# Kernel tuning notes

Hardware: AMD Instinct MI355X
Metric: run time of the kernel (lower is better)

## Reference

```python
import jax, jax.numpy as jnp
import numpy as np

D_MODEL = 1024
NHEAD = 16
HEAD_DIM = D_MODEL // NHEAD
MLP_DIM = 4096
ROPE_THETA = 10000.0


def layer_norm(x, g, b, eps=1e-5):
    mu = jnp.mean(x, axis=-1, keepdims=True)
    var = jnp.var(x, axis=-1, keepdims=True)
    return (x - mu) * jax.lax.rsqrt(var + eps) * g + b


def rope_cos_sin(seq_len, dim):
    # lucidrains RotaryEmbedding: inv_freq over even indices, freqs repeated interleaved
    inv_freq = 1.0 / (ROPE_THETA ** (jnp.arange(0, dim, 2, dtype=jnp.float32) / dim))
    t = jnp.arange(seq_len, dtype=jnp.float32)
    freqs = t[:, None] * inv_freq[None, :]            # (S, dim/2)
    freqs = jnp.repeat(freqs, 2, axis=-1)             # (S, dim) interleaved [f0,f0,f1,f1,...]
    return jnp.cos(freqs), jnp.sin(freqs)


def apply_rope(x, cos, sin):
    # x: (B, S, H, D); interleaved rotate_half: (x0,x1) -> (-x1, x0)
    x1 = x[..., ::2]
    x2 = x[..., 1::2]
    rot = jnp.stack([-x2, x1], axis=-1).reshape(x.shape)
    c = cos[None, :, None, :]
    s = sin[None, :, None, :]
    return x * c + rot * s


def setup_inputs() -> dict:
    key = jax.random.key(0)
    ks = jax.random.split(key, 8)
    B, S = 2, 2048
    sc = 1.0 / np.sqrt(D_MODEL)
    inputs = jax.random.normal(ks[0], (B, S, D_MODEL), dtype=jnp.float32)
    return {
        "inputs": inputs,
        "ln1_g": jnp.ones((D_MODEL,), jnp.float32),
        "ln1_b": jnp.zeros((D_MODEL,), jnp.float32),
        "Wq": jax.random.normal(ks[1], (D_MODEL, D_MODEL), jnp.float32) * sc,
        "Wk": jax.random.normal(ks[2], (D_MODEL, D_MODEL), jnp.float32) * sc,
        "Wv": jax.random.normal(ks[3], (D_MODEL, D_MODEL), jnp.float32) * sc,
        "Wo": jax.random.normal(ks[4], (D_MODEL, D_MODEL), jnp.float32) * sc,
        "ln2_g": jnp.ones((D_MODEL,), jnp.float32),
        "ln2_b": jnp.zeros((D_MODEL,), jnp.float32),
        "Wfc2": jax.random.normal(ks[5], (D_MODEL, MLP_DIM), jnp.float32) * sc,
        "bfc2": jnp.zeros((MLP_DIM,), jnp.float32),
        "Wfc3": jax.random.normal(ks[6], (MLP_DIM, D_MODEL), jnp.float32) * (1.0 / np.sqrt(MLP_DIM)),
        "bfc3": jnp.zeros((D_MODEL,), jnp.float32),
    }


def reference(inputs, ln1_g, ln1_b, Wq, Wk, Wv, Wo, ln2_g, ln2_b, Wfc2, bfc2, Wfc3, bfc3):
    B, S, _ = inputs.shape
    x = layer_norm(inputs, ln1_g, ln1_b)
    q = (x @ Wq).reshape(B, S, NHEAD, HEAD_DIM)
    k = (x @ Wk).reshape(B, S, NHEAD, HEAD_DIM)
    v = (x @ Wv).reshape(B, S, NHEAD, HEAD_DIM)
    cos, sin = rope_cos_sin(S, HEAD_DIM)
    q = apply_rope(q, cos, sin)
    k = apply_rope(k, cos, sin)
    scores = jnp.einsum('bqhd,bkhd->bhqk', q, k) / np.sqrt(HEAD_DIM)
    attn = jax.nn.softmax(scores, axis=-1)
    out = jnp.einsum('bhqk,bkhd->bqhd', attn, v).reshape(B, S, D_MODEL)
    out = out @ Wo
    mlp_in = out + inputs
    h = layer_norm(mlp_in, ln2_g, ln2_b)
    h = jax.nn.gelu(h @ Wfc2 + bfc2, approximate=False)
    h = h @ Wfc3 + bfc3
    return h + mlp_in
```

## Files before the change

kernel.cpp:

```cpp
#include <hip/hip_runtime.h>
#include <cstdint>
#include <cstddef>

typedef __bf16 bf16x8 __attribute__((ext_vector_type(8)));
typedef __bf16 bf16x4 __attribute__((ext_vector_type(4)));
typedef float  f32x4  __attribute__((ext_vector_type(4)));
typedef float  f32x16 __attribute__((ext_vector_type(16)));

__device__ __forceinline__ void load16_to_lds(const void* g, void* l) {
  __builtin_amdgcn_global_load_lds(
      (const __attribute__((address_space(1))) void*)g,
      (__attribute__((address_space(3))) void*)l, 16, 0, 0);
}

__global__ __launch_bounds__(256) void transpose_cast(
    const float* __restrict__ src, __bf16* __restrict__ dst, int K, int N)
{
  __shared__ float tile[32][33];
  const int n0 = blockIdx.x * 32, k0 = blockIdx.y * 32;
  const int tx = threadIdx.x, ty = threadIdx.y;
#pragma unroll
  for (int i = 0; i < 32; i += 8)
    tile[ty + i][tx] = src[(size_t)(k0 + ty + i) * N + n0 + tx];
  __syncthreads();
#pragma unroll
  for (int i = 0; i < 32; i += 8)
    dst[(size_t)(n0 + ty + i) * K + k0 + tx] = (__bf16)tile[tx][ty + i];
}

__global__ __launch_bounds__(256) void ln_kernel(
    const float* __restrict__ x, const float* __restrict__ g,
    const float* __restrict__ bta, __bf16* __restrict__ out)
{
  const int row = blockIdx.x;
  const int t = threadIdx.x;
  const float4 v = ((const float4*)(x + (size_t)row * 1024))[t];
  float s  = v.x + v.y + v.z + v.w;
  float ss = v.x * v.x + v.y * v.y + v.z * v.z + v.w * v.w;
#pragma unroll
  for (int o = 32; o > 0; o >>= 1) { s += __shfl_down(s, o); ss += __shfl_down(ss, o); }
  __shared__ float rs[4], rss[4];
  const int w = t >> 6, l = t & 63;
  if (l == 0) { rs[w] = s; rss[w] = ss; }
  __syncthreads();
  s  = rs[0] + rs[1] + rs[2] + rs[3];
  ss = rss[0] + rss[1] + rss[2] + rss[3];
  const float mu = s * (1.0f / 1024.0f);
  const float var = ss * (1.0f / 1024.0f) - mu * mu;
  const float rstd = rsqrtf(var + 1e-5f);
  const float4 gg = ((const float4*)g)[t];
  const float4 bb = ((const float4*)bta)[t];
  __bf16* o = out + (size_t)row * 1024 + t * 4;
  o[0] = (__bf16)((v.x - mu) * rstd * gg.x + bb.x);
  o[1] = (__bf16)((v.y - mu) * rstd * gg.y + bb.y);
  o[2] = (__bf16)((v.z - mu) * rstd * gg.z + bb.z);
  o[3] = (__bf16)((v.w - mu) * rstd * gg.w + bb.w);
}

enum { EPI_BF16 = 0, EPI_RES_F32 = 1, EPI_GELU_BF16 = 2, EPI_BIAS_RES_F32 = 3 };

template <int TM, int EPI>
__global__ __launch_bounds__(256, 2) void gemm_bf16(
    const __bf16* __restrict__ A, const __bf16* __restrict__ Bt,
    __bf16* __restrict__ outb, float* __restrict__ outf,
    const float* __restrict__ bias, const float* __restrict__ res,
    int M, int N, int K)
{
  constexpr int MT = TM / 32;
  __shared__ __bf16 As[TM * 32];
  __shared__ __bf16 Bs[128 * 32];
  const int tid  = threadIdx.x;
  const int lane = tid & 63, w = tid >> 6;
  const int wm = w >> 1, wn = w & 1;
  const int quad = lane >> 4, l16 = lane & 15;
  const int m0 = blockIdx.y * TM, n0 = blockIdx.x * 128;

  f32x4 acc[MT][4] = {};
  const __bf16* Ag = A  + (size_t)m0 * K;
  const __bf16* Bg = Bt + (size_t)n0 * K;

  for (int k0 = 0; k0 < K; k0 += 32) {
#pragma unroll
    for (int r = 0; r < TM / 64; ++r) {
      const int c = r * 256 + tid;
      const int row = c >> 2, cc = (c & 3) * 8;
      load16_to_lds(Ag + (size_t)row * K + k0 + cc, &As[c * 8]);
    }
#pragma unroll
    for (int r = 0; r < 2; ++r) {
      const int c = r * 256 + tid;
      const int row = c >> 2, cc = (c & 3) * 8;
      load16_to_lds(Bg + (size_t)row * K + k0 + cc, &Bs[c * 8]);
    }
    __syncthreads();
    bf16x8 af[MT], bfr[4];
#pragma unroll
    for (int mt = 0; mt < MT; ++mt)
      af[mt] = *(const bf16x8*)&As[(wm * (TM / 2) + mt * 16 + l16) * 32 + quad * 8];
#pragma unroll
    for (int nt = 0; nt < 4; ++nt)
      bfr[nt] = *(const bf16x8*)&Bs[(wn * 64 + nt * 16 + l16) * 32 + quad * 8];
#pragma unroll
    for (int mt = 0; mt < MT; ++mt)
#pragma unroll
      for (int nt = 0; nt < 4; ++nt)
        acc[mt][nt] = __builtin_amdgcn_mfma_f32_16x16x32_bf16(af[mt], bfr[nt], acc[mt][nt], 0, 0, 0);
    __syncthreads();
  }

#pragma unroll
  for (int mt = 0; mt < MT; ++mt) {
#pragma unroll
    for (int nt = 0; nt < 4; ++nt) {
      const int col = n0 + wn * 64 + nt * 16 + l16;
#pragma unroll
      for (int i = 0; i < 4; ++i) {
        const int row = m0 + wm * (TM / 2) + mt * 16 + quad * 4 + i;
        float v = acc[mt][nt][i];
        const size_t idx = (size_t)row * N + col;
        if (EPI == EPI_BF16) {
          outb[idx] = (__bf16)v;
        } else if (EPI == EPI_RES_F32) {
          outf[idx] = v + res[idx];
        } else if (EPI == EPI_GELU_BF16) {
          v += bias[col];
          outb[idx] = (__bf16)(0.5f * v * (1.0f + erff(v * 0.70710678118f)));
        } else {
          v += bias[col];
          outf[idx] = v + res[idx];
        }
      }
    }
  }
}

__global__ __launch_bounds__(256) void rope_qk(
    const __bf16* __restrict__ qkv, __bf16* __restrict__ qr, __bf16* __restrict__ kr)
{
  const int idx = blockIdx.x * 256 + threadIdx.x;
  const int d2 = idx & 31;
  const int h  = (idx >> 5) & 15;
  const int bs = idx >> 9;
  const int s  = bs & 2047;
  const int b  = bs >> 11;
  const float inv_freq = exp2f(-((float)d2 * (1.0f / 32.0f)) * 13.2877123795f);
  const float ang = (float)s * inv_freq;
  const float c = cosf(ang), sn = sinf(ang);
  const __bf16* qp = qkv + (size_t)bs * 3072 + h * 64 + 2 * d2;
  const __bf16* kp = qp + 1024;
  const float q0 = (float)qp[0], q1 = (float)qp[1];
  const float k0 = (float)kp[0], k1 = (float)kp[1];
  const size_t o = ((size_t)(b * 16 + h) * 2048 + s) * 64 + 2 * d2;
  qr[o]     = (__bf16)(q0 * c - q1 * sn);
  qr[o + 1] = (__bf16)(q1 * c + q0 * sn);
  kr[o]     = (__bf16)(k0 * c - k1 * sn);
  kr[o + 1] = (__bf16)(k1 * c + k0 * sn);
}

__global__ __launch_bounds__(256) void v_transpose(
    const __bf16* __restrict__ qkv, __bf16* __restrict__ vt)
{
  __shared__ __bf16 t[64][72];
  const int st = blockIdx.x, h = blockIdx.y, b = blockIdx.z;
  const int tx = threadIdx.x & 63, ty = threadIdx.x >> 6;
  const int s0 = st * 64;
  const __bf16* src = qkv + ((size_t)(b * 2048 + s0)) * 3072 + 2048 + h * 64;
#pragma unroll
  for (int i = 0; i < 64; i += 4)
    t[ty + i][tx] = src[(size_t)(ty + i) * 3072 + tx];
  __syncthreads();
  __bf16* dst = vt + ((size_t)(b * 16 + h) * 64) * 2048 + s0;
#pragma unroll
  for (int i = 0; i < 64; i += 4)
    dst[(size_t)(ty + i) * 2048 + tx] = t[tx][ty + i];
}

__global__ __launch_bounds__(256, 2) void attn_kernel(
    const __bf16* __restrict__ qr, const __bf16* __restrict__ kr,
    const __bf16* __restrict__ vt, __bf16* __restrict__ attn_o)
{
  constexpr int S = 2048, DH = 64, NH = 16, BQ = 128, BKK = 64;
  __shared__ __align__(16) __bf16 smem[24576];
  __bf16* Qs   = smem;
  __bf16* Ksb  = smem + 8192;
  __bf16* Vtsb = smem + 16384;

  const int tid = threadIdx.x;
  const int lane = tid & 63, w = tid >> 6;
  const int l32 = lane & 31, half = lane >> 5;
  const int qt = blockIdx.x, h = blockIdx.y, b = blockIdx.z;
  const int bh = b * NH + h;
  const __bf16* Q  = qr + ((size_t)bh * S + qt * BQ) * DH;
  const __bf16* Kp = kr + (size_t)bh * S * DH;
  const __bf16* Vp = vt + (size_t)bh * DH * S;
  __bf16* Pb = Qs + w * 2048;

#pragma unroll
  for (int r4 = 0; r4 < 4; ++r4) {
    const int c = r4 * 256 + tid;
    const int r = c >> 3, cb = c & 7;
    load16_to_lds(Q + (size_t)r * DH + ((cb ^ (r & 7)) * 8), &Qs[c * 8]);
  }
#pragma unroll
  for (int r2 = 0; r2 < 2; ++r2) {
    const int c = r2 * 256 + tid;
    const int r = c >> 3, cb = c & 7;
    const int cg = (cb ^ (r & 7)) * 8;
    load16_to_lds(Kp + (size_t)r * DH + cg, &Ksb[c * 8]);
    load16_to_lds(Vp + (size_t)r * S + cg, &Vtsb[c * 8]);
  }
  __syncthreads();

  bf16x8 qfB[4];
  {
    const int row = w * 32 + l32;
#pragma unroll
    for (int c = 0; c < 4; ++c)
      qfB[c] = *(const bf16x8*)&Qs[row * 64 + (((2 * c + half) ^ (row & 7)) * 8)];
  }

  float mreg = -3.0e38f, lreg = 0.0f;
  f32x16 oacc[2] = {};

  for (int kt = 0; kt < S / BKK; ++kt) {
    if (kt) __syncthreads();
    const __bf16* Ks  = Ksb  + (kt & 1) * 4096;
    const __bf16* Vts = Vtsb + (kt & 1) * 4096;

    bf16x8 kf[2][4], vf[2][4];
#pragma unroll
    for (int t = 0; t < 2; ++t) {
      const int row = 32 * t + l32;
#pragma unroll
      for (int c = 0; c < 4; ++c)
        kf[t][c] = *(const bf16x8*)&Ks[row * 64 + (((2 * c + half) ^ (l32 & 7)) * 8)];
    }
#pragma unroll
    for (int v = 0; v < 2; ++v) {
      const int row = 32 * v + l32;
#pragma unroll
      for (int c = 0; c < 4; ++c)
        vf[v][c] = *(const bf16x8*)&Vts[row * 64 + (((2 * c + half) ^ (l32 & 7)) * 8)];
    }

    if (kt + 1 < S / BKK) {
      __bf16* Kn = Ksb  + ((kt + 1) & 1) * 4096;
      __bf16* Vn = Vtsb + ((kt + 1) & 1) * 4096;
      const size_t kk1 = (size_t)(kt + 1) * BKK;
#pragma unroll
      for (int r2 = 0; r2 < 2; ++r2) {
        const int c = r2 * 256 + tid;
        const int r = c >> 3, cb = c & 7;
        const int cg = (cb ^ (r & 7)) * 8;
        load16_to_lds(Kp + (kk1 + r) * DH + cg, &Kn[c * 8]);
        load16_to_lds(Vp + (size_t)r * S + kk1 + cg, &Vn[c * 8]);
      }
    }

    f32x16 sa[2] = {};
#pragma unroll
    for (int t = 0; t < 2; ++t)
#pragma unroll
      for (int c = 0; c < 4; ++c)
        sa[t] = __builtin_amdgcn_mfma_f32_32x32x16_bf16(kf[t][c], qfB[c], sa[t], 0, 0, 0);

    float mx = -3.0e38f;
#pragma unroll
    for (int t = 0; t < 2; ++t)
#pragma unroll
      for (int r = 0; r < 16; ++r) { sa[t][r] *= 0.125f; mx = fmaxf(mx, sa[t][r]); }
    mx = fmaxf(mx, __shfl_xor(mx, 32));
    const float mnew = fmaxf(mreg, mx);
    const float alpha = __expf(mreg - mnew);
    mreg = mnew;
    float sum = 0.0f;
#pragma unroll
    for (int t = 0; t < 2; ++t)
#pragma unroll
      for (int r = 0; r < 16; ++r) {
        const float p = __expf(sa[t][r] - mnew);
        sa[t][r] = p;
        sum += p;
      }
    sum += __shfl_xor(sum, 32);
    lreg = lreg * alpha + sum;
#pragma unroll
    for (int v = 0; v < 2; ++v)
#pragma unroll
      for (int r = 0; r < 16; ++r) oacc[v][r] *= alpha;

#pragma unroll
    for (int t = 0; t < 2; ++t)
#pragma unroll
      for (int g = 0; g < 4; ++g) {
        bf16x4 pv;
#pragma unroll
        for (int i = 0; i < 4; ++i) pv[i] = (__bf16)sa[t][4 * g + i];
        const int kc = 4 * t + g;
        *(bf16x4*)&Pb[l32 * 64 + ((kc ^ (l32 & 7)) * 8) + 4 * half] = pv;
      }

    bf16x8 pf[4];
#pragma unroll
    for (int c = 0; c < 4; ++c)
      pf[c] = *(const bf16x8*)&Pb[l32 * 64 + (((2 * c + half) ^ (l32 & 7)) * 8)];
#pragma unroll
    for (int v = 0; v < 2; ++v)
#pragma unroll
      for (int c = 0; c < 4; ++c)
        oacc[v] = __builtin_amdgcn_mfma_f32_32x32x16_bf16(vf[v][c], pf[c], oacc[v], 0, 0, 0);
  }

  const float linv = 1.0f / lreg;
#pragma unroll
  for (int v = 0; v < 2; ++v)
#pragma unroll
    for (int g = 0; g < 4; ++g) {
      bf16x4 ov;
#pragma unroll
      for (int i = 0; i < 4; ++i) ov[i] = (__bf16)(oacc[v][4 * g + i] * linv);
      const int dc = 4 * v + g;
      *(bf16x4*)&Pb[l32 * 64 + ((dc ^ (l32 & 7)) * 8) + 4 * half] = ov;
    }
#pragma unroll
  for (int cc = 0; cc < 4; ++cc) {
    const int c = cc * 64 + lane;
    const int r = c >> 3, g = c & 7;
    const bf16x8 od = *(const bf16x8*)&Pb[r * 64 + ((g ^ (r & 7)) * 8)];
    const int srow = qt * BQ + w * 32 + r;
    *(bf16x8*)&attn_o[((size_t)b * S + srow) * 1024 + h * 64 + g * 8] = od;
  }
}

extern "C" void kernel_launch(void* const* d_in, const int* in_sizes, int n_in,
                              void* d_out, int out_size, void* d_ws, size_t ws_size,
                              hipStream_t stream) {
  const float* inputs = (const float*)d_in[0];
  const float* ln1_g  = (const float*)d_in[1];
  const float* ln1_b  = (const float*)d_in[2];
  const float* Wq     = (const float*)d_in[3];
  const float* Wk     = (const float*)d_in[4];
  const float* Wv     = (const float*)d_in[5];
  const float* Wo     = (const float*)d_in[6];
  const float* ln2_g  = (const float*)d_in[7];
  const float* ln2_b  = (const float*)d_in[8];
  const float* Wfc2   = (const float*)d_in[9];
  const float* bfc2   = (const float*)d_in[10];
  const float* Wfc3   = (const float*)d_in[11];
  const float* bfc3   = (const float*)d_in[12];
  float* out = (float*)d_out;
  char* ws = (char*)d_ws;
  const size_t MB = 1024 * 1024;

  __bf16* Wqkv_t = (__bf16*)(ws);
  __bf16* Wo_t   = (__bf16*)(ws + 6 * MB);
  __bf16* Wfc2_t = (__bf16*)(ws + 8 * MB);
  __bf16* Wfc3_t = (__bf16*)(ws + 16 * MB);
  __bf16* xb     = (__bf16*)(ws + 24 * MB);
  __bf16* attn_o = xb;
  __bf16* qkv    = (__bf16*)(ws + 32 * MB);
  float*  mlp_in = (float*)(ws + 32 * MB);
  __bf16* h2     = (__bf16*)(ws + 48 * MB);
  __bf16* qrb    = (__bf16*)(ws + 56 * MB);
  __bf16* krb    = (__bf16*)(ws + 64 * MB);
  __bf16* vtb    = (__bf16*)(ws + 72 * MB);
  __bf16* hbuf   = (__bf16*)(ws + 56 * MB);

  const dim3 tb(32, 8);
  transpose_cast<<<dim3(32, 32),  tb, 0, stream>>>(Wq,   Wqkv_t,                1024, 1024);
  transpose_cast<<<dim3(32, 32),  tb, 0, stream>>>(Wk,   Wqkv_t + 1024 * 1024,  1024, 1024);
  transpose_cast<<<dim3(32, 32),  tb, 0, stream>>>(Wv,   Wqkv_t + 2048 * 1024,  1024, 1024);
  transpose_cast<<<dim3(32, 32),  tb, 0, stream>>>(Wo,   Wo_t,                  1024, 1024);
  transpose_cast<<<dim3(128, 32), tb, 0, stream>>>(Wfc2, Wfc2_t,                1024, 4096);
  transpose_cast<<<dim3(32, 128), tb, 0, stream>>>(Wfc3, Wfc3_t,                4096, 1024);

  ln_kernel<<<4096, 256, 0, stream>>>(inputs, ln1_g, ln1_b, xb);

  gemm_bf16<128, EPI_BF16><<<dim3(24, 32), 256, 0, stream>>>(
      xb, Wqkv_t, qkv, nullptr, nullptr, nullptr, 4096, 3072, 1024);

  rope_qk<<<8192, 256, 0, stream>>>(qkv, qrb, krb);
  v_transpose<<<dim3(32, 16, 2), 256, 0, stream>>>(qkv, vtb);

  attn_kernel<<<dim3(16, 16, 2), 256, 0, stream>>>(qrb, krb, vtb, attn_o);

  gemm_bf16<64, EPI_RES_F32><<<dim3(8, 64), 256, 0, stream>>>(
      attn_o, Wo_t, nullptr, mlp_in, nullptr, inputs, 4096, 1024, 1024);

  ln_kernel<<<4096, 256, 0, stream>>>(mlp_in, ln2_g, ln2_b, h2);

  gemm_bf16<128, EPI_GELU_BF16><<<dim3(32, 32), 256, 0, stream>>>(
      h2, Wfc2_t, hbuf, nullptr, bfc2, nullptr, 4096, 4096, 1024);

  gemm_bf16<64, EPI_BIAS_RES_F32><<<dim3(8, 64), 256, 0, stream>>>(
      hbuf, Wfc3_t, nullptr, out, bfc3, mlp_in, 4096, 1024, 4096);
}
```

Before: 393.1 us.

## Split-K the narrow-N GEMMs with atomic accumulation and merge QKV weight transposes

The Wo and FC3 projections (N=1024) now run split-K (2 and 4 ways) across a z grid dimension. Partial sums are atomically added into an output that a new init kernel pre-fills with the residual (plus bias for FC3). The QKV GEMM moves to 64-row tiles to double the number of blocks, and the three QKV weight transposes become one launch. The aim is better CU occupancy on the small-grid GEMMs and fewer launches, at the cost of extra init passes, atomic traffic and nondeterministic summation order.

```diff
diff --git a/kernel.cpp b/kernel.cpp
--- a/kernel.cpp
+++ b/kernel.cpp
@@ -26,6 +26,37 @@
 #pragma unroll
   for (int i = 0; i < 32; i += 8)
     dst[(size_t)(n0 + ty + i) * K + k0 + tx] = (__bf16)tile[tx][ty + i];
+}
+
+__global__ __launch_bounds__(256) void transpose_cast_qkv(
+    const float* __restrict__ s0, const float* __restrict__ s1,
+    const float* __restrict__ s2, __bf16* __restrict__ dst)
+{
+  __shared__ float tile[32][33];
+  const float* src = blockIdx.z == 0 ? s0 : blockIdx.z == 1 ? s1 : s2;
+  __bf16* d = dst + (size_t)blockIdx.z * 1024 * 1024;
+  const int n0 = blockIdx.x * 32, k0 = blockIdx.y * 32;
+  const int tx = threadIdx.x, ty = threadIdx.y;
+#pragma unroll
+  for (int i = 0; i < 32; i += 8)
+    tile[ty + i][tx] = src[(size_t)(k0 + ty + i) * 1024 + n0 + tx];
+  __syncthreads();
+#pragma unroll
+  for (int i = 0; i < 32; i += 8)
+    d[(size_t)(n0 + ty + i) * 1024 + k0 + tx] = (__bf16)tile[tx][ty + i];
+}
+
+__global__ __launch_bounds__(256) void init_out(
+    const float* __restrict__ a, const float* __restrict__ bias,
+    float* __restrict__ o)
+{
+  const int i = blockIdx.x * 256 + threadIdx.x;
+  float4 v = ((const float4*)a)[i];
+  if (bias != nullptr) {
+    const float4 bb = ((const float4*)bias)[i & 255];
+    v.x += bb.x; v.y += bb.y; v.z += bb.z; v.w += bb.w;
+  }
+  ((float4*)o)[i] = v;
 }
 
 __global__ __launch_bounds__(256) void ln_kernel(
@@ -57,9 +88,9 @@
   o[3] = (__bf16)((v.w - mu) * rstd * gg.w + bb.w);
 }
 
-enum { EPI_BF16 = 0, EPI_RES_F32 = 1, EPI_GELU_BF16 = 2, EPI_BIAS_RES_F32 = 3 };
-
-template <int TM, int EPI>
+enum { EPI_BF16 = 0, EPI_RES_F32 = 1, EPI_GELU_BF16 = 2, EPI_ATOMIC = 3 };
+
+template <int TM, int SK, int EPI>
 __global__ __launch_bounds__(256, 2) void gemm_bf16(
     const __bf16* __restrict__ A, const __bf16* __restrict__ Bt,
     __bf16* __restrict__ outb, float* __restrict__ outf,
@@ -74,12 +105,14 @@
   const int wm = w >> 1, wn = w & 1;
   const int quad = lane >> 4, l16 = lane & 15;
   const int m0 = blockIdx.y * TM, n0 = blockIdx.x * 128;
+  const int Ks = K / SK;
+  const int kbase = blockIdx.z * Ks;
 
   f32x4 acc[MT][4] = {};
-  const __bf16* Ag = A  + (size_t)m0 * K;
-  const __bf16* Bg = Bt + (size_t)n0 * K;
-
-  for (int k0 = 0; k0 < K; k0 += 32) {
+  const __bf16* Ag = A  + (size_t)m0 * K + kbase;
+  const __bf16* Bg = Bt + (size_t)n0 * K + kbase;
+
+  for (int k0 = 0; k0 < Ks; k0 += 32) {
 #pragma unroll
     for (int r = 0; r < TM / 64; ++r) {
       const int c = r * 256 + tid;
@@ -126,8 +159,7 @@
           v += bias[col];
           outb[idx] = (__bf16)(0.5f * v * (1.0f + erff(v * 0.70710678118f)));
         } else {
-          v += bias[col];
-          outf[idx] = v + res[idx];
+          atomicAdd(&outf[idx], v);
         }
       }
     }
@@ -367,16 +399,14 @@
   __bf16* hbuf   = (__bf16*)(ws + 56 * MB);
 
   const dim3 tb(32, 8);
-  transpose_cast<<<dim3(32, 32),  tb, 0, stream>>>(Wq,   Wqkv_t,                1024, 1024);
-  transpose_cast<<<dim3(32, 32),  tb, 0, stream>>>(Wk,   Wqkv_t + 1024 * 1024,  1024, 1024);
-  transpose_cast<<<dim3(32, 32),  tb, 0, stream>>>(Wv,   Wqkv_t + 2048 * 1024,  1024, 1024);
-  transpose_cast<<<dim3(32, 32),  tb, 0, stream>>>(Wo,   Wo_t,                  1024, 1024);
-  transpose_cast<<<dim3(128, 32), tb, 0, stream>>>(Wfc2, Wfc2_t,                1024, 4096);
-  transpose_cast<<<dim3(32, 128), tb, 0, stream>>>(Wfc3, Wfc3_t,                4096, 1024);
+  transpose_cast_qkv<<<dim3(32, 32, 3), tb, 0, stream>>>(Wq, Wk, Wv, Wqkv_t);
+  transpose_cast<<<dim3(32, 32),  tb, 0, stream>>>(Wo,   Wo_t,   1024, 1024);
+  transpose_cast<<<dim3(128, 32), tb, 0, stream>>>(Wfc2, Wfc2_t, 1024, 4096);
+  transpose_cast<<<dim3(32, 128), tb, 0, stream>>>(Wfc3, Wfc3_t, 4096, 1024);
 
   ln_kernel<<<4096, 256, 0, stream>>>(inputs, ln1_g, ln1_b, xb);
 
-  gemm_bf16<128, EPI_BF16><<<dim3(24, 32), 256, 0, stream>>>(
+  gemm_bf16<64, 1, EPI_BF16><<<dim3(24, 64), 256, 0, stream>>>(
       xb, Wqkv_t, qkv, nullptr, nullptr, nullptr, 4096, 3072, 1024);
 
   rope_qk<<<8192, 256, 0, stream>>>(qkv, qrb, krb);
@@ -384,14 +414,16 @@
 
   attn_kernel<<<dim3(16, 16, 2), 256, 0, stream>>>(qrb, krb, vtb, attn_o);
 
-  gemm_bf16<64, EPI_RES_F32><<<dim3(8, 64), 256, 0, stream>>>(
-      attn_o, Wo_t, nullptr, mlp_in, nullptr, inputs, 4096, 1024, 1024);
+  init_out<<<4096, 256, 0, stream>>>(inputs, nullptr, mlp_in);
+  gemm_bf16<64, 2, EPI_ATOMIC><<<dim3(8, 64, 2), 256, 0, stream>>>(
+      attn_o, Wo_t, nullptr, mlp_in, nullptr, nullptr, 4096, 1024, 1024);
 
   ln_kernel<<<4096, 256, 0, stream>>>(mlp_in, ln2_g, ln2_b, h2);
 
-  gemm_bf16<128, EPI_GELU_BF16><<<dim3(32, 32), 256, 0, stream>>>(
+  gemm_bf16<128, 1, EPI_GELU_BF16><<<dim3(32, 32), 256, 0, stream>>>(
       h2, Wfc2_t, hbuf, nullptr, bfc2, nullptr, 4096, 4096, 1024);
 
-  gemm_bf16<64, EPI_BIAS_RES_F32><<<dim3(8, 64), 256, 0, stream>>>(
-      hbuf, Wfc3_t, nullptr, out, bfc3, mlp_in, 4096, 1024, 4096);
-}
+  init_out<<<4096, 256, 0, stream>>>(mlp_in, bfc3, out);
+  gemm_bf16<64, 4, EPI_ATOMIC><<<dim3(8, 64, 4), 256, 0, stream>>>(
+      hbuf, Wfc3_t, nullptr, out, nullptr, nullptr, 4096, 1024, 4096);
+}
```

New measurement: 441.1 us. +12.2%, slower.

## Double-buffer GEMM LDS tiles, merge QKV weight transposes, shrink QKV tile

Applied to the files above, without the earlier changes.

The GEMM kernel now uses two LDS buffers per operand. It prefetches the next K tile via global_load_lds while issuing MFMAs on the current one, and drops one barrier per iteration. The three Q/K/V weight transpose-casts are merged into one launch using blockIdx.z. The QKV projection switches to 64-row tiles with twice the blocks. Double buffering doubles LDS per block, which may reduce occupancy, and the single barrier relies on the async LDS loads being complete when it is reached.

```diff
diff --git a/kernel.cpp b/kernel.cpp
--- a/kernel.cpp
+++ b/kernel.cpp
@@ -26,6 +26,24 @@
 #pragma unroll
   for (int i = 0; i < 32; i += 8)
     dst[(size_t)(n0 + ty + i) * K + k0 + tx] = (__bf16)tile[tx][ty + i];
+}
+
+__global__ __launch_bounds__(256) void transpose_cast_qkv(
+    const float* __restrict__ s0, const float* __restrict__ s1,
+    const float* __restrict__ s2, __bf16* __restrict__ dst)
+{
+  __shared__ float tile[32][33];
+  const float* src = blockIdx.z == 0 ? s0 : blockIdx.z == 1 ? s1 : s2;
+  __bf16* d = dst + (size_t)blockIdx.z * 1024 * 1024;
+  const int n0 = blockIdx.x * 32, k0 = blockIdx.y * 32;
+  const int tx = threadIdx.x, ty = threadIdx.y;
+#pragma unroll
+  for (int i = 0; i < 32; i += 8)
+    tile[ty + i][tx] = src[(size_t)(k0 + ty + i) * 1024 + n0 + tx];
+  __syncthreads();
+#pragma unroll
+  for (int i = 0; i < 32; i += 8)
+    d[(size_t)(n0 + ty + i) * 1024 + k0 + tx] = (__bf16)tile[tx][ty + i];
 }
 
 __global__ __launch_bounds__(256) void ln_kernel(
@@ -67,8 +85,8 @@
     int M, int N, int K)
 {
   constexpr int MT = TM / 32;
-  __shared__ __bf16 As[TM * 32];
-  __shared__ __bf16 Bs[128 * 32];
+  __shared__ __bf16 As[2][TM * 32];
+  __shared__ __bf16 Bs[2][128 * 32];
   const int tid  = threadIdx.x;
   const int lane = tid & 63, w = tid >> 6;
   const int wm = w >> 1, wn = w & 1;
@@ -79,33 +97,53 @@
   const __bf16* Ag = A  + (size_t)m0 * K;
   const __bf16* Bg = Bt + (size_t)n0 * K;
 
-  for (int k0 = 0; k0 < K; k0 += 32) {
-#pragma unroll
-    for (int r = 0; r < TM / 64; ++r) {
-      const int c = r * 256 + tid;
-      const int row = c >> 2, cc = (c & 3) * 8;
-      load16_to_lds(Ag + (size_t)row * K + k0 + cc, &As[c * 8]);
-    }
-#pragma unroll
-    for (int r = 0; r < 2; ++r) {
-      const int c = r * 256 + tid;
-      const int row = c >> 2, cc = (c & 3) * 8;
-      load16_to_lds(Bg + (size_t)row * K + k0 + cc, &Bs[c * 8]);
-    }
+#pragma unroll
+  for (int r = 0; r < TM / 64; ++r) {
+    const int c = r * 256 + tid;
+    const int row = c >> 2, cc = (c & 3) * 8;
+    load16_to_lds(Ag + (size_t)row * K + cc, &As[0][c * 8]);
+  }
+#pragma unroll
+  for (int r = 0; r < 2; ++r) {
+    const int c = r * 256 + tid;
+    const int row = c >> 2, cc = (c & 3) * 8;
+    load16_to_lds(Bg + (size_t)row * K + cc, &Bs[0][c * 8]);
+  }
+
+  const int nk = K >> 5;
+  for (int kt = 0; kt < nk; ++kt) {
     __syncthreads();
+    const int p = kt & 1;
+
     bf16x8 af[MT], bfr[4];
 #pragma unroll
     for (int mt = 0; mt < MT; ++mt)
-      af[mt] = *(const bf16x8*)&As[(wm * (TM / 2) + mt * 16 + l16) * 32 + quad * 8];
+      af[mt] = *(const bf16x8*)&As[p][(wm * (TM / 2) + mt * 16 + l16) * 32 + quad * 8];
 #pragma unroll
     for (int nt = 0; nt < 4; ++nt)
-      bfr[nt] = *(const bf16x8*)&Bs[(wn * 64 + nt * 16 + l16) * 32 + quad * 8];
+      bfr[nt] = *(const bf16x8*)&Bs[p][(wn * 64 + nt * 16 + l16) * 32 + quad * 8];
+
+    if (kt + 1 < nk) {
+      const int k1 = (kt + 1) * 32;
+#pragma unroll
+      for (int r = 0; r < TM / 64; ++r) {
+        const int c = r * 256 + tid;
+        const int row = c >> 2, cc = (c & 3) * 8;
+        load16_to_lds(Ag + (size_t)row * K + k1 + cc, &As[1 - p][c * 8]);
+      }
+#pragma unroll
+      for (int r = 0; r < 2; ++r) {
+        const int c = r * 256 + tid;
+        const int row = c >> 2, cc = (c & 3) * 8;
+        load16_to_lds(Bg + (size_t)row * K + k1 + cc, &Bs[1 - p][c * 8]);
+      }
+    }
+
 #pragma unroll
     for (int mt = 0; mt < MT; ++mt)
 #pragma unroll
       for (int nt = 0; nt < 4; ++nt)
         acc[mt][nt] = __builtin_amdgcn_mfma_f32_16x16x32_bf16(af[mt], bfr[nt], acc[mt][nt], 0, 0, 0);
-    __syncthreads();
   }
 
 #pragma unroll
@@ -367,16 +405,14 @@
   __bf16* hbuf   = (__bf16*)(ws + 56 * MB);
 
   const dim3 tb(32, 8);
-  transpose_cast<<<dim3(32, 32),  tb, 0, stream>>>(Wq,   Wqkv_t,                1024, 1024);
-  transpose_cast<<<dim3(32, 32),  tb, 0, stream>>>(Wk,   Wqkv_t + 1024 * 1024,  1024, 1024);
-  transpose_cast<<<dim3(32, 32),  tb, 0, stream>>>(Wv,   Wqkv_t + 2048 * 1024,  1024, 1024);
-  transpose_cast<<<dim3(32, 32),  tb, 0, stream>>>(Wo,   Wo_t,                  1024, 1024);
-  transpose_cast<<<dim3(128, 32), tb, 0, stream>>>(Wfc2, Wfc2_t,                1024, 4096);
-  transpose_cast<<<dim3(32, 128), tb, 0, stream>>>(Wfc3, Wfc3_t,                4096, 1024);
+  transpose_cast_qkv<<<dim3(32, 32, 3), tb, 0, stream>>>(Wq, Wk, Wv, Wqkv_t);
+  transpose_cast<<<dim3(32, 32),  tb, 0, stream>>>(Wo,   Wo_t,   1024, 1024);
+  transpose_cast<<<dim3(128, 32), tb, 0, stream>>>(Wfc2, Wfc2_t, 1024, 4096);
+  transpose_cast<<<dim3(32, 128), tb, 0, stream>>>(Wfc3, Wfc3_t, 4096, 1024);
 
   ln_kernel<<<4096, 256, 0, stream>>>(inputs, ln1_g, ln1_b, xb);
 
-  gemm_bf16<128, EPI_BF16><<<dim3(24, 32), 256, 0, stream>>>(
+  gemm_bf16<64, EPI_BF16><<<dim3(24, 64), 256, 0, stream>>>(
       xb, Wqkv_t, qkv, nullptr, nullptr, nullptr, 4096, 3072, 1024);
 
   rope_qk<<<8192, 256, 0, stream>>>(qkv, qrb, krb);
```

Result: faster. 383.3 us (-2.5%).
